# Optimization experiments

Measured on AMD Instinct MI355X. Metric: run time of the kernel, lower is better.

Reference implementation:

```python
import jax, jax.numpy as jnp
import numpy as np

# Cell hyperparameters (from model.cell / Eprop_fit.__init__)
THRESHOLD = 0.6
DAMPENING = 0.3
N_REF = 5
DECAY = 0.8          # membrane decay used for pre-synaptic trace filters
ELIG_DECAY = 0.8     # default decay in exp_convolve for eligibility filtering
REG = 300.0


def exp_convolve(t, decay):
    """Causal exponential filter along time axis 1: a_t = decay*a_{t-1} + x_t."""
    xt = jnp.moveaxis(t, 1, 0)  # time-major [T, B, ...]

    def step(acc, cur):
        acc = acc * decay + cur
        return acc, acc

    _, y = jax.lax.scan(step, jnp.zeros_like(xt[0]), xt)
    return jnp.moveaxis(y, 0, 1)


def refractory_count(z, n_ref):
    """ref_count[t] depends on z[:t]; starts at 0."""
    zt = jnp.moveaxis(jax.lax.stop_gradient(z), 1, 0)  # [T, B, N]
    init = jnp.zeros(zt.shape[1:], jnp.int32)

    def step(c, zc):
        c = jnp.where(zc > 0, jnp.int32(n_ref - 1), jnp.maximum(0, c - 1))
        return c, c

    _, counts = jax.lax.scan(step, init, zt[:-1])
    counts = jnp.concatenate([init[None], counts], axis=0)
    return jnp.moveaxis(counts, 0, 1)  # [B, T, N]


def setup_inputs() -> dict:
    key = jax.random.key(0)
    k1, k2, k3, k4, k5, k6 = jax.random.split(key, 6)
    B, T, N, NIN, K = 4, 300, 200, 100, 10
    v = jax.random.normal(k1, (B, T, N), jnp.float32) * 0.5 + 0.3
    z = (jax.random.uniform(k2, (B, T, N)) < 0.05).astype(jnp.float32)  # spikes
    x = (jax.random.uniform(k3, (B, T, NIN)) < 0.1).astype(jnp.float32)
    error1 = jax.random.normal(k4, (B, T, K), jnp.float32) * 0.1   # output error
    error2 = jax.random.normal(k5, (N,), jnp.float32) * 0.01       # firing-rate error
    w_out = jax.random.normal(k6, (N, K), jnp.float32) / np.sqrt(N)
    return {"v": v, "z": z, "x": x, "error1": error1, "error2": error2, "w_out": w_out}


def reference(v, z, x, error1, error2, w_out):
    B, T, N = v.shape

    v_scaled = (v - THRESHOLD) / THRESHOLD
    psi_no_ref = DAMPENING * jnp.maximum(1.0 - jnp.abs(v_scaled), 0.0) / THRESHOLD

    ref = refractory_count(z, N_REF)
    post_term = jnp.where(ref > 0, 0.0, psi_no_ref)  # [B, T, N]

    # shift z by one time step (z_{t-1}, zero-initialized)
    z_prev = jnp.concatenate([jnp.zeros_like(z[:, :1]), z[:, :-1]], axis=1)

    pre_w_in = exp_convolve(x, DECAY)        # x_bar  [B, T, n_in]
    pre_w_rec = exp_convolve(z_prev, DECAY)  # z_bar  [B, T, N]
    pre_w_out = exp_convolve(z, DECAY)       # [B, T, N]

    # eligibility traces: [B, T, pre, post]
    et_in = post_term[:, :, None, :] * pre_w_in[:, :, :, None]
    et_rec = post_term[:, :, None, :] * pre_w_rec[:, :, :, None]

    fet_in = exp_convolve(et_in, ELIG_DECAY)
    fet_rec = exp_convolve(et_rec, ELIG_DECAY)

    avg_in = jnp.mean(et_in, axis=(0, 1))    # [n_in, N]
    avg_rec = jnp.mean(et_rec, axis=(0, 1))  # [N, N]

    # learning signals (symmetric e-prop): L = error @ w_out^T
    learning_signals = jnp.einsum('btk,jk->btj', error1, w_out)  # [B, T, N]

    dloss_dw_out = jnp.einsum('btk,btj->jk', error1, pre_w_out)          # [N, K]
    dloss_dw_in = jnp.einsum('btj,btij->ij', learning_signals, fet_in)   # [n_in, N]
    dloss_dw_rec = jnp.einsum('btj,btij->ij', learning_signals, fet_rec) # [N, N]

    dloss_dw_in = dloss_dw_in + REG * (error2 * avg_in)
    dloss_dw_rec = dloss_dw_rec + REG * (error2 * avg_rec)

    # mask autapses (diagonal of recurrent weight gradient)
    eye = jnp.eye(N, dtype=bool)
    dloss_dw_rec = jnp.where(eye, 0.0, dloss_dw_rec)

    return dloss_dw_in, dloss_dw_rec, dloss_dw_out
```

## Files before the change

### kernel.cpp

```cpp
#include <hip/hip_runtime.h>

#define BB    4
#define TT    300
#define NN    200
#define NINN  100
#define KK    10
#define DECAY 0.8f
#define THR   0.6f
#define DAMP  0.3f

#define LCH   20
#define NCHK  (TT / LCH)
#define WARM  48

#define XBAR_OFF  0
#define ZFILT_OFF (BB*TT*NINN)
#define ZBAR_OFF  (ZFILT_OFF + BB*TT*NN)
#define CBUF_OFF  (ZBAR_OFF  + BB*TT*NN)
#define GBAR_OFF  (CBUF_OFF  + BB*TT*NN)

#define R_A_N     (BB*NCHK*NINN)
#define R_B_BASE  6144
#define R_B_N     (BB*NCHK*NN)
#define R_G_BASE  18176
#define R_G_N     (BB*NCHK*KK)
#define R_Z_BASE  18944
#define R_Z_N     500
#define K1_TOTAL  (R_Z_BASE + R_Z_N)

__global__ void scan_kernel(const float* __restrict__ z,
                            const float* __restrict__ x,
                            const float* __restrict__ error1,
                            float* __restrict__ ws,
                            float* __restrict__ out) {
    int tid = blockIdx.x * blockDim.x + threadIdx.x;
    float* xbar  = ws + XBAR_OFF;
    float* zfilt = ws + ZFILT_OFF;
    float* zbar  = ws + ZBAR_OFF;
    float* gbar  = ws + GBAR_OFF;

    if (tid < R_A_N) {
        int i = tid % NINN, r = tid / NINN;
        int chunk = r % NCHK, b = r / NCHK;
        int t0 = chunk * LCH;
        const float* src = x + (size_t)b * TT * NINN + i;
        float acc = 0.f;
        #pragma unroll
        for (int d = WARM; d >= 1; --d) {
            int t = t0 - d;
            int tc = t < 0 ? 0 : t;
            float val = src[tc * NINN];
            acc = DECAY * acc + (t < 0 ? 0.f : val);
        }
        float vals[LCH];
        #pragma unroll
        for (int tt = 0; tt < LCH; ++tt) vals[tt] = src[(t0 + tt) * NINN];
        #pragma unroll
        for (int tt = 0; tt < LCH; ++tt) { acc = DECAY * acc + vals[tt]; vals[tt] = acc; }
        float* dst = xbar + (size_t)b * TT * NINN + i;
        #pragma unroll
        for (int tt = 0; tt < LCH; ++tt) dst[(t0 + tt) * NINN] = vals[tt];
    } else if (tid >= R_B_BASE && tid < R_B_BASE + R_B_N) {
        int u = tid - R_B_BASE;
        int j = u % NN, r = u / NN;
        int chunk = r % NCHK, b = r / NCHK;
        int t0 = chunk * LCH;
        const float* src = z + (size_t)b * TT * NN + j;
        float acc = 0.f;
        #pragma unroll
        for (int d = WARM; d >= 1; --d) {
            int t = t0 - d;
            int tc = t < 0 ? 0 : t;
            float val = src[tc * NN];
            acc = DECAY * acc + (t < 0 ? 0.f : val);
        }
        float zv[LCH], pre[LCH];
        #pragma unroll
        for (int tt = 0; tt < LCH; ++tt) zv[tt] = src[(t0 + tt) * NN];
        #pragma unroll
        for (int tt = 0; tt < LCH; ++tt) {
            pre[tt] = acc;
            acc = DECAY * acc + zv[tt];
            zv[tt] = acc;
        }
        float* dzb = zbar  + (size_t)b * TT * NN + j;
        float* dzf = zfilt + (size_t)b * TT * NN + j;
        #pragma unroll
        for (int tt = 0; tt < LCH; ++tt) dzb[(t0 + tt) * NN] = pre[tt];
        #pragma unroll
        for (int tt = 0; tt < LCH; ++tt) dzf[(t0 + tt) * NN] = zv[tt];
    } else if (tid >= R_G_BASE && tid < R_G_BASE + R_G_N) {
        int u = tid - R_G_BASE;
        int k = u % KK, r = u / KK;
        int chunk = r % NCHK, b = r / NCHK;
        int t0 = chunk * LCH, t1 = t0 + LCH - 1;
        const float* src = error1 + (size_t)b * TT * KK + k;
        float G = 0.f;
        #pragma unroll
        for (int d = WARM; d >= 1; --d) {
            int t = t1 + d;
            int tc = t > TT - 1 ? TT - 1 : t;
            float val = src[tc * KK];
            G = DECAY * G + (t > TT - 1 ? 0.f : val);
        }
        float ev[LCH];
        #pragma unroll
        for (int tt = 0; tt < LCH; ++tt) ev[tt] = src[(t1 - tt) * KK];
        float* dst = gbar + (size_t)b * TT * KK + k;
        #pragma unroll
        for (int tt = 0; tt < LCH; ++tt) {
            G = DECAY * G + ev[tt];
            dst[(t1 - tt) * KK] = G;
        }
    } else if (tid >= R_Z_BASE && tid < R_Z_BASE + R_Z_N) {
        int u = tid - R_Z_BASE;
        ((float4*)(out + NINN * NN + NN * NN))[u] = make_float4(0.f, 0.f, 0.f, 0.f);
    }
}

__global__ void c_kernel(const float* __restrict__ v,
                         const float* __restrict__ z,
                         const float* __restrict__ error2,
                         const float* __restrict__ w_out,
                         float* __restrict__ ws) {
    int tid = blockIdx.x * blockDim.x + threadIdx.x;
    if (tid >= BB * TT * NN / 4) return;
    const float* gbar = ws + GBAR_OFF;
    float* cbuf = ws + CBUF_OFF;

    int jq = tid % (NN / 4), bt = tid / (NN / 4);
    int j0 = jq * 4;
    int t = bt % TT, b = bt / TT;

    float g[KK];
    #pragma unroll
    for (int k = 0; k < KK; ++k) g[k] = gbar[bt * KK + k];

    float Ld[4];
    #pragma unroll
    for (int a = 0; a < 4; ++a) {
        const float* wr = w_out + (j0 + a) * KK;
        float acc = 0.f;
        #pragma unroll
        for (int k = 0; k < KK; ++k) acc += g[k] * wr[k];
        Ld[a] = acc;
    }

    float4 e2 = *(const float4*)(error2 + j0);
    float co[4] = {0.25f * e2.x, 0.25f * e2.y, 0.25f * e2.z, 0.25f * e2.w};

    bool refr[4] = {false, false, false, false};
    #pragma unroll
    for (int d = 1; d <= 4; ++d) {
        int s = t - d;
        int sc = s < 0 ? 0 : s;
        float4 zv = *(const float4*)(z + ((size_t)b * TT + sc) * NN + j0);
        if (s >= 0) {
            if (zv.x > 0.f) refr[0] = true;
            if (zv.y > 0.f) refr[1] = true;
            if (zv.z > 0.f) refr[2] = true;
            if (zv.w > 0.f) refr[3] = true;
        }
    }

    float4 vv = *(const float4*)(v + (size_t)bt * NN + j0);
    float vm[4] = {vv.x, vv.y, vv.z, vv.w};
    float cm[4];
    #pragma unroll
    for (int a = 0; a < 4; ++a) {
        float vs = (vm[a] - THR) / THR;
        float psi = (DAMP / THR) * fmaxf(1.f - fabsf(vs), 0.f);
        cm[a] = (refr[a] ? 0.f : psi) * (Ld[a] + co[a]);
    }
    *(float4*)(cbuf + (size_t)bt * NN + j0) = make_float4(cm[0], cm[1], cm[2], cm[3]);
}

#define SKB 16
#define KC3 (BB * TT / SKB)
#define PT  4
#define JT  64

__global__ void out_kernel(const float* __restrict__ error1,
                           const float* __restrict__ ws,
                           float* __restrict__ out) {
    __shared__ float red[SKB * PT * JT];
    int bid = blockIdx.x;
    int tid = threadIdx.x;
    const float* xbar  = ws + XBAR_OFF;
    const float* zfilt = ws + ZFILT_OFF;
    const float* zbar  = ws + ZBAR_OFF;
    const float* cbuf  = ws + CBUF_OFF;

    if (bid < 300) {
        int pt = bid >> 2;
        int jt = bid & 3;
        int p0 = pt * PT;
        int j0 = jt * JT;
        int W = NN - j0; if (W > JT) W = JT;
        int jq = tid & 15;
        int s  = tid >> 4;

        if (jq * 4 < W) {
            bool isrec = (p0 >= NINN);
            const float* A = isrec ? (zbar + (p0 - NINN)) : (xbar + p0);
            int lda = isrec ? NN : NINN;
            const float* C = cbuf + j0 + jq * 4;
            int bt0 = s * KC3;
            float acc[4][4];
            #pragma unroll
            for (int a = 0; a < 4; ++a)
                #pragma unroll
                for (int c = 0; c < 4; ++c) acc[a][c] = 0.f;
            #pragma unroll 5
            for (int rr = 0; rr < KC3; ++rr) {
                int bt = bt0 + rr;
                float4 av = *(const float4*)(A + (size_t)bt * lda);
                float4 cv = *(const float4*)(C + (size_t)bt * NN);
                float am[4] = {av.x, av.y, av.z, av.w};
                float cm[4] = {cv.x, cv.y, cv.z, cv.w};
                #pragma unroll
                for (int a = 0; a < 4; ++a)
                    #pragma unroll
                    for (int c = 0; c < 4; ++c) acc[a][c] += am[a] * cm[c];
            }
            float* dst = red + s * (PT * JT) + jq * 4;
            #pragma unroll
            for (int a = 0; a < 4; ++a)
                *(float4*)(dst + a * JT) =
                    make_float4(acc[a][0], acc[a][1], acc[a][2], acc[a][3]);
        }
        __syncthreads();

        int o = tid;
        int pl = o >> 6, jl = o & 63;
        if (jl < W) {
            float sum = 0.f;
            #pragma unroll
            for (int s2 = 0; s2 < SKB; ++s2) sum += red[s2 * (PT * JT) + o];
            int row = p0 + pl;
            int j = j0 + jl;
            if (row < NINN) {
                out[row * NN + j] = sum;
            } else {
                int i = row - NINN;
                out[NINN * NN + i * NN + j] = (i == j) ? 0.f : sum;
            }
        }
    } else {
        int u = (bid - 300) * 256 + tid;
        if (u < 6 * NN * KK) {
            int jk = u % (NN * KK);
            int s = u / (NN * KK);
            int j = jk % NN;
            int k = jk / NN;
            int bt0 = s * 200;
            float acc = 0.f;
            #pragma unroll 8
            for (int rr = 0; rr < 200; ++rr) {
                int bt = bt0 + rr;
                acc += zfilt[bt * NN + j] * error1[bt * KK + k];
            }
            atomicAdd(out + NINN * NN + NN * NN + j * KK + k, acc);
        }
    }
}

extern "C" void kernel_launch(void* const* d_in, const int* in_sizes, int n_in,
                              void* d_out, int out_size, void* d_ws, size_t ws_size,
                              hipStream_t stream) {
    const float* v  = (const float*)d_in[0];
    const float* z  = (const float*)d_in[1];
    const float* x  = (const float*)d_in[2];
    const float* e1 = (const float*)d_in[3];
    const float* e2 = (const float*)d_in[4];
    const float* wo = (const float*)d_in[5];
    float* out = (float*)d_out;
    float* ws  = (float*)d_ws;

    scan_kernel<<<(K1_TOTAL + 255) / 256, 256, 0, stream>>>(z, x, e1, ws, out);

    c_kernel<<<(BB * TT * NN / 4 + 255) / 256, 256, 0, stream>>>(v, z, e2, wo, ws);

    out_kernel<<<347, 256, 0, stream>>>(e1, ws, out);
}
```

Baseline: 87.54 us.

## Fuse scan and c-term kernels into one launch with local reverse error filter

Merges the scan kernel and the c-term kernel into a single block-partitioned launch. The reverse-filtered error (gbar) is no longer written to workspace. Instead, each c-term block recomputes it directly from error1 with a truncated 48-step window into shared memory. This removes one kernel launch and the global round trip for gbar, at the cost of redundant per-block error filtering.

```diff
diff --git a/kernel.cpp b/kernel.cpp
--- a/kernel.cpp
+++ b/kernel.cpp
@@ -17,162 +17,158 @@
 #define ZFILT_OFF (BB*TT*NINN)
 #define ZBAR_OFF  (ZFILT_OFF + BB*TT*NN)
 #define CBUF_OFF  (ZBAR_OFF  + BB*TT*NN)
-#define GBAR_OFF  (CBUF_OFF  + BB*TT*NN)
-
-#define R_A_N     (BB*NCHK*NINN)
-#define R_B_BASE  6144
-#define R_B_N     (BB*NCHK*NN)
-#define R_G_BASE  18176
-#define R_G_N     (BB*NCHK*KK)
-#define R_Z_BASE  18944
-#define R_Z_N     500
-#define K1_TOTAL  (R_Z_BASE + R_Z_N)
-
-__global__ void scan_kernel(const float* __restrict__ z,
-                            const float* __restrict__ x,
-                            const float* __restrict__ error1,
-                            float* __restrict__ ws,
-                            float* __restrict__ out) {
-    int tid = blockIdx.x * blockDim.x + threadIdx.x;
+
+#define NB_A 24
+#define NB_B 47
+#define NB_C 240
+#define CB_BASE  (NB_A + NB_B)
+#define ZB_BASE  (CB_BASE + NB_C)
+#define NB_TOTAL (ZB_BASE + 2)
+
+__global__ void fused_kernel(const float* __restrict__ v,
+                             const float* __restrict__ z,
+                             const float* __restrict__ x,
+                             const float* __restrict__ error1,
+                             const float* __restrict__ error2,
+                             const float* __restrict__ w_out,
+                             float* __restrict__ ws,
+                             float* __restrict__ out) {
+    int bid = blockIdx.x;
+    int tid = threadIdx.x;
     float* xbar  = ws + XBAR_OFF;
     float* zfilt = ws + ZFILT_OFF;
     float* zbar  = ws + ZBAR_OFF;
-    float* gbar  = ws + GBAR_OFF;
-
-    if (tid < R_A_N) {
-        int i = tid % NINN, r = tid / NINN;
-        int chunk = r % NCHK, b = r / NCHK;
-        int t0 = chunk * LCH;
-        const float* src = x + (size_t)b * TT * NINN + i;
-        float acc = 0.f;
-        #pragma unroll
-        for (int d = WARM; d >= 1; --d) {
-            int t = t0 - d;
-            int tc = t < 0 ? 0 : t;
-            float val = src[tc * NINN];
-            acc = DECAY * acc + (t < 0 ? 0.f : val);
-        }
-        float vals[LCH];
-        #pragma unroll
-        for (int tt = 0; tt < LCH; ++tt) vals[tt] = src[(t0 + tt) * NINN];
-        #pragma unroll
-        for (int tt = 0; tt < LCH; ++tt) { acc = DECAY * acc + vals[tt]; vals[tt] = acc; }
-        float* dst = xbar + (size_t)b * TT * NINN + i;
-        #pragma unroll
-        for (int tt = 0; tt < LCH; ++tt) dst[(t0 + tt) * NINN] = vals[tt];
-    } else if (tid >= R_B_BASE && tid < R_B_BASE + R_B_N) {
-        int u = tid - R_B_BASE;
-        int j = u % NN, r = u / NN;
-        int chunk = r % NCHK, b = r / NCHK;
-        int t0 = chunk * LCH;
-        const float* src = z + (size_t)b * TT * NN + j;
-        float acc = 0.f;
-        #pragma unroll
-        for (int d = WARM; d >= 1; --d) {
-            int t = t0 - d;
-            int tc = t < 0 ? 0 : t;
-            float val = src[tc * NN];
-            acc = DECAY * acc + (t < 0 ? 0.f : val);
-        }
-        float zv[LCH], pre[LCH];
-        #pragma unroll
-        for (int tt = 0; tt < LCH; ++tt) zv[tt] = src[(t0 + tt) * NN];
-        #pragma unroll
-        for (int tt = 0; tt < LCH; ++tt) {
-            pre[tt] = acc;
-            acc = DECAY * acc + zv[tt];
-            zv[tt] = acc;
-        }
-        float* dzb = zbar  + (size_t)b * TT * NN + j;
-        float* dzf = zfilt + (size_t)b * TT * NN + j;
-        #pragma unroll
-        for (int tt = 0; tt < LCH; ++tt) dzb[(t0 + tt) * NN] = pre[tt];
-        #pragma unroll
-        for (int tt = 0; tt < LCH; ++tt) dzf[(t0 + tt) * NN] = zv[tt];
-    } else if (tid >= R_G_BASE && tid < R_G_BASE + R_G_N) {
-        int u = tid - R_G_BASE;
-        int k = u % KK, r = u / KK;
-        int chunk = r % NCHK, b = r / NCHK;
-        int t0 = chunk * LCH, t1 = t0 + LCH - 1;
-        const float* src = error1 + (size_t)b * TT * KK + k;
-        float G = 0.f;
-        #pragma unroll
-        for (int d = WARM; d >= 1; --d) {
-            int t = t1 + d;
-            int tc = t > TT - 1 ? TT - 1 : t;
-            float val = src[tc * KK];
-            G = DECAY * G + (t > TT - 1 ? 0.f : val);
-        }
-        float ev[LCH];
-        #pragma unroll
-        for (int tt = 0; tt < LCH; ++tt) ev[tt] = src[(t1 - tt) * KK];
-        float* dst = gbar + (size_t)b * TT * KK + k;
-        #pragma unroll
-        for (int tt = 0; tt < LCH; ++tt) {
-            G = DECAY * G + ev[tt];
-            dst[(t1 - tt) * KK] = G;
-        }
-    } else if (tid >= R_Z_BASE && tid < R_Z_BASE + R_Z_N) {
-        int u = tid - R_Z_BASE;
-        ((float4*)(out + NINN * NN + NN * NN))[u] = make_float4(0.f, 0.f, 0.f, 0.f);
+    float* cbuf  = ws + CBUF_OFF;
+
+    if (bid < NB_A) {
+        int u = bid * 256 + tid;
+        if (u < BB * NCHK * NINN) {
+            int i = u % NINN, r = u / NINN;
+            int chunk = r % NCHK, b = r / NCHK;
+            int t0 = chunk * LCH;
+            const float* src = x + (size_t)b * TT * NINN + i;
+            float acc = 0.f;
+            #pragma unroll
+            for (int d = WARM; d >= 1; --d) {
+                int t = t0 - d;
+                int tc = t < 0 ? 0 : t;
+                float val = src[tc * NINN];
+                acc = DECAY * acc + (t < 0 ? 0.f : val);
+            }
+            float vals[LCH];
+            #pragma unroll
+            for (int tt = 0; tt < LCH; ++tt) vals[tt] = src[(t0 + tt) * NINN];
+            #pragma unroll
+            for (int tt = 0; tt < LCH; ++tt) { acc = DECAY * acc + vals[tt]; vals[tt] = acc; }
+            float* dst = xbar + (size_t)b * TT * NINN + i;
+            #pragma unroll
+            for (int tt = 0; tt < LCH; ++tt) dst[(t0 + tt) * NINN] = vals[tt];
+        }
+    } else if (bid < CB_BASE) {
+        int u = (bid - NB_A) * 256 + tid;
+        if (u < BB * NCHK * NN) {
+            int j = u % NN, r = u / NN;
+            int chunk = r % NCHK, b = r / NCHK;
+            int t0 = chunk * LCH;
+            const float* src = z + (size_t)b * TT * NN + j;
+            float acc = 0.f;
+            #pragma unroll
+            for (int d = WARM; d >= 1; --d) {
+                int t = t0 - d;
+                int tc = t < 0 ? 0 : t;
+                float val = src[tc * NN];
+                acc = DECAY * acc + (t < 0 ? 0.f : val);
+            }
+            float zv[LCH], pre[LCH];
+            #pragma unroll
+            for (int tt = 0; tt < LCH; ++tt) zv[tt] = src[(t0 + tt) * NN];
+            #pragma unroll
+            for (int tt = 0; tt < LCH; ++tt) {
+                pre[tt] = acc;
+                acc = DECAY * acc + zv[tt];
+                zv[tt] = acc;
+            }
+            float* dzb = zbar  + (size_t)b * TT * NN + j;
+            float* dzf = zfilt + (size_t)b * TT * NN + j;
+            #pragma unroll
+            for (int tt = 0; tt < LCH; ++tt) dzb[(t0 + tt) * NN] = pre[tt];
+            #pragma unroll
+            for (int tt = 0; tt < LCH; ++tt) dzf[(t0 + tt) * NN] = zv[tt];
+        }
+    } else if (bid < ZB_BASE) {
+        __shared__ float gl[5][KK];
+        int cb = bid - CB_BASE;
+        int bt0 = cb * 5;
+        int b = bt0 / TT;
+        int t0 = bt0 - b * TT;
+        if (tid < 5 * KK) {
+            int btl = tid / KK, k = tid - btl * KK;
+            int t = t0 + btl;
+            const float* src = error1 + (size_t)b * TT * KK + k;
+            float G = 0.f;
+            #pragma unroll
+            for (int d = WARM - 1; d >= 0; --d) {
+                int s = t + d;
+                int sc = s > TT - 1 ? TT - 1 : s;
+                float val = src[sc * KK];
+                G = DECAY * G + (s > TT - 1 ? 0.f : val);
+            }
+            gl[btl][k] = G;
+        }
+        __syncthreads();
+        if (tid < 250) {
+            int jq = tid % 50, btl = tid / 50;
+            int t = t0 + btl;
+            int bt = bt0 + btl;
+            int j0 = jq * 4;
+
+            float g[KK];
+            #pragma unroll
+            for (int k = 0; k < KK; ++k) g[k] = gl[btl][k];
+
+            float Ld[4];
+            #pragma unroll
+            for (int a = 0; a < 4; ++a) {
+                const float* wr = w_out + (j0 + a) * KK;
+                float acc = 0.f;
+                #pragma unroll
+                for (int k = 0; k < KK; ++k) acc += g[k] * wr[k];
+                Ld[a] = acc;
+            }
+
+            float4 e2v = *(const float4*)(error2 + j0);
+            float co[4] = {0.25f * e2v.x, 0.25f * e2v.y, 0.25f * e2v.z, 0.25f * e2v.w};
+
+            bool refr[4] = {false, false, false, false};
+            #pragma unroll
+            for (int d = 1; d <= 4; ++d) {
+                int s = t - d;
+                int sc = s < 0 ? 0 : s;
+                float4 zv = *(const float4*)(z + ((size_t)b * TT + sc) * NN + j0);
+                if (s >= 0) {
+                    if (zv.x > 0.f) refr[0] = true;
+                    if (zv.y > 0.f) refr[1] = true;
+                    if (zv.z > 0.f) refr[2] = true;
+                    if (zv.w > 0.f) refr[3] = true;
+                }
+            }
+
+            float4 vv = *(const float4*)(v + (size_t)bt * NN + j0);
+            float vm[4] = {vv.x, vv.y, vv.z, vv.w};
+            float cm[4];
+            #pragma unroll
+            for (int a = 0; a < 4; ++a) {
+                float vs = (vm[a] - THR) / THR;
+                float psi = (DAMP / THR) * fmaxf(1.f - fabsf(vs), 0.f);
+                cm[a] = (refr[a] ? 0.f : psi) * (Ld[a] + co[a]);
+            }
+            *(float4*)(cbuf + (size_t)bt * NN + j0) = make_float4(cm[0], cm[1], cm[2], cm[3]);
+        }
+    } else {
+        int u = (bid - ZB_BASE) * 256 + tid;
+        if (u < 500)
+            ((float4*)(out + NINN * NN + NN * NN))[u] = make_float4(0.f, 0.f, 0.f, 0.f);
     }
-}
-
-__global__ void c_kernel(const float* __restrict__ v,
-                         const float* __restrict__ z,
-                         const float* __restrict__ error2,
-                         const float* __restrict__ w_out,
-                         float* __restrict__ ws) {
-    int tid = blockIdx.x * blockDim.x + threadIdx.x;
-    if (tid >= BB * TT * NN / 4) return;
-    const float* gbar = ws + GBAR_OFF;
-    float* cbuf = ws + CBUF_OFF;
-
-    int jq = tid % (NN / 4), bt = tid / (NN / 4);
-    int j0 = jq * 4;
-    int t = bt % TT, b = bt / TT;
-
-    float g[KK];
-    #pragma unroll
-    for (int k = 0; k < KK; ++k) g[k] = gbar[bt * KK + k];
-
-    float Ld[4];
-    #pragma unroll
-    for (int a = 0; a < 4; ++a) {
-        const float* wr = w_out + (j0 + a) * KK;
-        float acc = 0.f;
-        #pragma unroll
-        for (int k = 0; k < KK; ++k) acc += g[k] * wr[k];
-        Ld[a] = acc;
-    }
-
-    float4 e2 = *(const float4*)(error2 + j0);
-    float co[4] = {0.25f * e2.x, 0.25f * e2.y, 0.25f * e2.z, 0.25f * e2.w};
-
-    bool refr[4] = {false, false, false, false};
-    #pragma unroll
-    for (int d = 1; d <= 4; ++d) {
-        int s = t - d;
-        int sc = s < 0 ? 0 : s;
-        float4 zv = *(const float4*)(z + ((size_t)b * TT + sc) * NN + j0);
-        if (s >= 0) {
-            if (zv.x > 0.f) refr[0] = true;
-            if (zv.y > 0.f) refr[1] = true;
-            if (zv.z > 0.f) refr[2] = true;
-            if (zv.w > 0.f) refr[3] = true;
-        }
-    }
-
-    float4 vv = *(const float4*)(v + (size_t)bt * NN + j0);
-    float vm[4] = {vv.x, vv.y, vv.z, vv.w};
-    float cm[4];
-    #pragma unroll
-    for (int a = 0; a < 4; ++a) {
-        float vs = (vm[a] - THR) / THR;
-        float psi = (DAMP / THR) * fmaxf(1.f - fabsf(vs), 0.f);
-        cm[a] = (refr[a] ? 0.f : psi) * (Ld[a] + co[a]);
-    }
-    *(float4*)(cbuf + (size_t)bt * NN + j0) = make_float4(cm[0], cm[1], cm[2], cm[3]);
 }
 
 #define SKB 16
@@ -277,9 +273,7 @@
     float* out = (float*)d_out;
     float* ws  = (float*)d_ws;
 
-    scan_kernel<<<(K1_TOTAL + 255) / 256, 256, 0, stream>>>(z, x, e1, ws, out);
-
-    c_kernel<<<(BB * TT * NN / 4 + 255) / 256, 256, 0, stream>>>(v, z, e2, wo, ws);
+    fused_kernel<<<NB_TOTAL, 256, 0, stream>>>(v, z, x, e1, e2, wo, ws, out);
 
     out_kernel<<<347, 256, 0, stream>>>(e1, ws, out);
 }
```

Measured after the change: 85.56 us. 2.3% less time.
